# Optimization experiments

Measured on AMD Instinct MI355X. Metric: run time of the kernel, lower is better.

Reference implementation:

```python
import jax, jax.numpy as jnp
import numpy as np

B, AT, NBR, FEAT = 4, 384, 24, 128


def setup_inputs() -> dict:
    key = jax.random.key(0)
    k1, k2, k3 = jax.random.split(key, 3)
    edge_embedding = jax.random.normal(k1, (B, AT, NBR, FEAT), dtype=jnp.float32)
    nbr_idx = jax.random.randint(k2, (B, AT, NBR), 0, AT, dtype=jnp.int64)
    # periodic-cell offsets: small integers stored as float, compared exactly with ==
    cell_offset = jax.random.randint(k3, (B, AT, NBR, 3), 0, 3).astype(jnp.float32)
    return {"edge_embedding": edge_embedding, "nbr_idx": nbr_idx, "cell_offset": cell_offset}


def reference(edge_embedding, nbr_idx, cell_offset):
    # edge_embedding: (B, At, Nbr, F); nbr_idx: (B, At, Nbr) int; cell_offset: (B, At, Nbr, 3)
    Bn, At, Nbr, F = edge_embedding.shape

    # j_nbr[b,a,j,k] = nbr_idx[b, nbr_idx[b,a,j], k]  -- neighbors of atom j (j-th nbr of a)
    j_nbr = jax.vmap(lambda n: n[n])(nbr_idx)                      # (B, At, Nbr, Nbr)
    # cell_j[b,a,j,k,:] = cell_offset[b, nbr_idx[b,a,j], k, :]
    cell_j = jax.vmap(lambda c, n: c[n])(cell_offset, nbr_idx)     # (B, At, Nbr, Nbr, 3)

    # k_masked[b,a,j,i] = nbr_idx[b,a,i] with diagonal (i==j) set to -1 (exclude k==j)
    eye = jnp.eye(Nbr, dtype=bool)                                 # (Nbr, Nbr) [j, i]
    k_masked = jnp.where(eye[None, None], -1, nbr_idx[:, :, None, :])  # (B, At, Nbr, Nbr)

    # match over k: j_nbr[b,a,j,k] == k_masked[b,a,j,i]
    idx_eq = j_nbr[:, :, :, None, :] == k_masked[:, :, :, :, None]      # (B,At,Nbr,Nbr_i,Nbr_k)
    # cell check: cell_offset[b,a,i,:] == cell_j[b,a,j,k,:] for all 3 coords
    cell_eq = jnp.all(
        cell_offset[:, :, None, :, None, :] == cell_j[:, :, :, None, :, :],
        axis=-1,
    )                                                              # (B,At,Nbr,Nbr_i,Nbr_k)

    mask = jnp.any(idx_eq & cell_eq, axis=-1)                      # (B, At, Nbr_j, Nbr_i)

    # edge_jk[b,a,j,i,:] = edge_embedding[b,a,i,:] where mask else 0
    edge_jk = jnp.where(mask[..., None], edge_embedding[:, :, None, :, :],
                        jnp.zeros((), dtype=edge_embedding.dtype))
    return edge_jk
```

## Files before the change

### kernel.cpp

```cpp
#include <hip/hip_runtime.h>

#define Bb 4
#define AT 384
#define NBR 24
#define FEAT 128

__global__ __launch_bounds__(256) void GetEdgeJK_kernel(
    const float* __restrict__ edge,
    const int*   __restrict__ nbr,
    const float* __restrict__ cell,
    float*       __restrict__ out)
{
    const int blk = blockIdx.x;
    const int j   = blk % NBR;
    const int ba  = blk / NBR;
    const int b   = ba / AT;

    __shared__ int   s_nbrj[NBR];
    __shared__ float s_cellj[NBR][3];
    __shared__ int   s_mask[NBR];

    const int t = threadIdx.x;

    const int jatom = nbr[ba * NBR + j];

    if (t < NBR) {
        const int base = (b * AT + jatom) * NBR + t;
        s_nbrj[t]     = nbr[base];
        s_cellj[t][0] = cell[base * 3 + 0];
        s_cellj[t][1] = cell[base * 3 + 1];
        s_cellj[t][2] = cell[base * 3 + 2];
    }
    __syncthreads();

    if (t < NBR) {
        const int i = t;
        int m = 0;
        if (i != j) {
            const int   myidx = nbr[ba * NBR + i];
            const float c0 = cell[(ba * NBR + i) * 3 + 0];
            const float c1 = cell[(ba * NBR + i) * 3 + 1];
            const float c2 = cell[(ba * NBR + i) * 3 + 2];
            #pragma unroll
            for (int k = 0; k < NBR; ++k) {
                if (s_nbrj[k] == myidx &&
                    s_cellj[k][0] == c0 &&
                    s_cellj[k][1] == c1 &&
                    s_cellj[k][2] == c2) { m = 1; }
            }
        }
        s_mask[i] = m;
    }
    __syncthreads();

    const float4* __restrict__ erow = (const float4*)(edge + (size_t)ba * NBR * FEAT);
    float4*       __restrict__ orow = (float4*)(out + (size_t)blk * NBR * FEAT);

    const float4 zero = make_float4(0.f, 0.f, 0.f, 0.f);
    #pragma unroll
    for (int it = 0; it < 3; ++it) {
        const int q = t + it * 256;
        const int i = q >> 5;
        float4 v = zero;
        if (s_mask[i]) v = erow[q];
        orow[q] = v;
    }
}

extern "C" void kernel_launch(void* const* d_in, const int* in_sizes, int n_in,
                              void* d_out, int out_size, void* d_ws, size_t ws_size,
                              hipStream_t stream) {
    const float* edge = (const float*)d_in[0];
    const int*   nbr  = (const int*)d_in[1];
    const float* cell = (const float*)d_in[2];
    float*       out  = (float*)d_out;

    const int nblocks = Bb * AT * NBR;
    GetEdgeJK_kernel<<<nblocks, 256, 0, stream>>>(edge, nbr, cell, out);
}
```

Baseline: 88.31 us.

## Process all neighbor rows of an atom in one block to reuse loads

Changes the grid from one block per (atom, j) pair to one block per atom. Each block stages the atom's neighbor list, cell offsets and all second-hop neighbor data in shared memory, computes the full 24x24 mask, then writes all 24 output panels. This is meant to cut per-block launch and setup overhead and to reuse the edge rows across j. The cost is 24x fewer blocks with more serial work each, which lowers parallelism for what is a store-bound kernel.

```diff
diff --git a/kernel.cpp b/kernel.cpp
--- a/kernel.cpp
+++ b/kernel.cpp
@@ -4,77 +4,90 @@
 #define AT 384
 #define NBR 24
 #define FEAT 128
+#define ROWQ (FEAT / 4)
+#define PANELQ (NBR * ROWQ)
 
 __global__ __launch_bounds__(256) void GetEdgeJK_kernel(
-    const float* __restrict__ edge,
-    const int*   __restrict__ nbr,
-    const float* __restrict__ cell,
-    float*       __restrict__ out)
+    const float4* __restrict__ edge,
+    const int*    __restrict__ nbr,
+    const float*  __restrict__ cell,
+    float4*       __restrict__ out)
 {
-    const int blk = blockIdx.x;
-    const int j   = blk % NBR;
-    const int ba  = blk / NBR;
-    const int b   = ba / AT;
+    const int ba = blockIdx.x;
+    const int b  = ba / AT;
+    const int t  = threadIdx.x;
 
-    __shared__ int   s_nbrj[NBR];
-    __shared__ float s_cellj[NBR][3];
-    __shared__ int   s_mask[NBR];
-
-    const int t = threadIdx.x;
-
-    const int jatom = nbr[ba * NBR + j];
+    __shared__ int   s_nbr[NBR];
+    __shared__ float s_cell[NBR][3];
+    __shared__ int   s_nbrj[NBR][NBR];
+    __shared__ float s_cellj[NBR][NBR][3];
+    __shared__ int   s_mask[NBR * NBR];
 
     if (t < NBR) {
-        const int base = (b * AT + jatom) * NBR + t;
-        s_nbrj[t]     = nbr[base];
-        s_cellj[t][0] = cell[base * 3 + 0];
-        s_cellj[t][1] = cell[base * 3 + 1];
-        s_cellj[t][2] = cell[base * 3 + 2];
+        s_nbr[t]     = nbr[ba * NBR + t];
+        s_cell[t][0] = cell[(ba * NBR + t) * 3 + 0];
+        s_cell[t][1] = cell[(ba * NBR + t) * 3 + 1];
+        s_cell[t][2] = cell[(ba * NBR + t) * 3 + 2];
     }
     __syncthreads();
 
-    if (t < NBR) {
-        const int i = t;
-        int m = 0;
-        if (i != j) {
-            const int   myidx = nbr[ba * NBR + i];
-            const float c0 = cell[(ba * NBR + i) * 3 + 0];
-            const float c1 = cell[(ba * NBR + i) * 3 + 1];
-            const float c2 = cell[(ba * NBR + i) * 3 + 2];
-            #pragma unroll
-            for (int k = 0; k < NBR; ++k) {
-                if (s_nbrj[k] == myidx &&
-                    s_cellj[k][0] == c0 &&
-                    s_cellj[k][1] == c1 &&
-                    s_cellj[k][2] == c2) { m = 1; }
-            }
-        }
-        s_mask[i] = m;
+    for (int q = t; q < NBR * NBR; q += 256) {
+        const int j = q / NBR;
+        const int k = q % NBR;
+        const int base = (b * AT + s_nbr[j]) * NBR + k;
+        s_nbrj[j][k]     = nbr[base];
+        s_cellj[j][k][0] = cell[base * 3 + 0];
+        s_cellj[j][k][1] = cell[base * 3 + 1];
+        s_cellj[j][k][2] = cell[base * 3 + 2];
     }
     __syncthreads();
 
-    const float4* __restrict__ erow = (const float4*)(edge + (size_t)ba * NBR * FEAT);
-    float4*       __restrict__ orow = (float4*)(out + (size_t)blk * NBR * FEAT);
+    for (int p = t; p < NBR * NBR; p += 256) {
+        const int j = p / NBR;
+        const int i = p % NBR;
+        int m = 0;
+        if (i != j) {
+            const int   myidx = s_nbr[i];
+            const float c0 = s_cell[i][0];
+            const float c1 = s_cell[i][1];
+            const float c2 = s_cell[i][2];
+            #pragma unroll
+            for (int k = 0; k < NBR; ++k) {
+                if (s_nbrj[j][k] == myidx &&
+                    s_cellj[j][k][0] == c0 &&
+                    s_cellj[j][k][1] == c1 &&
+                    s_cellj[j][k][2] == c2) { m = 1; }
+            }
+        }
+        s_mask[p] = m;
+    }
+    __syncthreads();
 
+    const float4* __restrict__ erow = edge + (size_t)ba * PANELQ;
+    float4*       __restrict__ orow = out  + (size_t)ba * NBR * PANELQ;
     const float4 zero = make_float4(0.f, 0.f, 0.f, 0.f);
-    #pragma unroll
-    for (int it = 0; it < 3; ++it) {
-        const int q = t + it * 256;
-        const int i = q >> 5;
-        float4 v = zero;
-        if (s_mask[i]) v = erow[q];
-        orow[q] = v;
+
+    for (int j = 0; j < NBR; ++j) {
+        const int* __restrict__ mrow = &s_mask[j * NBR];
+        #pragma unroll
+        for (int it = 0; it < 3; ++it) {
+            const int q = it * 256 + t;
+            const int i = q >> 5;
+            float4 v = zero;
+            if (mrow[i]) v = erow[q];
+            orow[j * PANELQ + q] = v;
+        }
     }
 }
 
 extern "C" void kernel_launch(void* const* d_in, const int* in_sizes, int n_in,
                               void* d_out, int out_size, void* d_ws, size_t ws_size,
                               hipStream_t stream) {
-    const float* edge = (const float*)d_in[0];
-    const int*   nbr  = (const int*)d_in[1];
-    const float* cell = (const float*)d_in[2];
-    float*       out  = (float*)d_out;
+    const float4* edge = (const float4*)d_in[0];
+    const int*    nbr  = (const int*)d_in[1];
+    const float*  cell = (const float*)d_in[2];
+    float4*       out  = (float4*)d_out;
 
-    const int nblocks = Bb * AT * NBR;
+    const int nblocks = Bb * AT;
     GetEdgeJK_kernel<<<nblocks, 256, 0, stream>>>(edge, nbr, cell, out);
 }
```

New measurement: 100.3 us. +13.6%, slower.

## Split mask computation into separate kernel and use nontemporal bitmask-driven stores

Applied to the files above, without the earlier changes.

Computes the per-(atom, j) neighbor match mask once per atom in a dedicated kernel, packing it into a 24-bit word in workspace. A lean store kernel then reads one word and streams the output with nontemporal stores. This removes the dependent gather loads and two barriers from every output block. It adds an extra launch and a workspace round trip, and falls back to the fused kernel when workspace is insufficient.

```diff
diff --git a/kernel.cpp b/kernel.cpp
--- a/kernel.cpp
+++ b/kernel.cpp
@@ -4,8 +4,102 @@
 #define AT 384
 #define NBR 24
 #define FEAT 128
+#define ROWQ (FEAT / 4)
+#define PANELQ (NBR * ROWQ)
 
-__global__ __launch_bounds__(256) void GetEdgeJK_kernel(
+typedef float vfloat4 __attribute__((ext_vector_type(4)));
+
+__global__ __launch_bounds__(256) void mask_kernel(
+    const int*   __restrict__ nbr,
+    const float* __restrict__ cell,
+    unsigned int* __restrict__ ws)
+{
+    const int ba = blockIdx.x;
+    const int b  = ba / AT;
+    const int t  = threadIdx.x;
+
+    __shared__ int   s_nbr[NBR];
+    __shared__ float s_cell[NBR][3];
+    __shared__ int   s_nbrj[NBR][NBR];
+    __shared__ float s_cellj[NBR][NBR][3];
+    __shared__ int   s_mask[NBR * NBR];
+
+    if (t < NBR) {
+        s_nbr[t]     = nbr[ba * NBR + t];
+        s_cell[t][0] = cell[(ba * NBR + t) * 3 + 0];
+        s_cell[t][1] = cell[(ba * NBR + t) * 3 + 1];
+        s_cell[t][2] = cell[(ba * NBR + t) * 3 + 2];
+    }
+    __syncthreads();
+
+    for (int q = t; q < NBR * NBR; q += 256) {
+        const int j = q / NBR;
+        const int k = q % NBR;
+        const int base = (b * AT + s_nbr[j]) * NBR + k;
+        s_nbrj[j][k]     = nbr[base];
+        s_cellj[j][k][0] = cell[base * 3 + 0];
+        s_cellj[j][k][1] = cell[base * 3 + 1];
+        s_cellj[j][k][2] = cell[base * 3 + 2];
+    }
+    __syncthreads();
+
+    for (int p = t; p < NBR * NBR; p += 256) {
+        const int j = p / NBR;
+        const int i = p % NBR;
+        int m = 0;
+        if (i != j) {
+            const int   myidx = s_nbr[i];
+            const float c0 = s_cell[i][0];
+            const float c1 = s_cell[i][1];
+            const float c2 = s_cell[i][2];
+            #pragma unroll
+            for (int k = 0; k < NBR; ++k) {
+                if (s_nbrj[j][k] == myidx &&
+                    s_cellj[j][k][0] == c0 &&
+                    s_cellj[j][k][1] == c1 &&
+                    s_cellj[j][k][2] == c2) { m = 1; }
+            }
+        }
+        s_mask[p] = m;
+    }
+    __syncthreads();
+
+    if (t < NBR) {
+        const int j = t;
+        unsigned int w = 0;
+        #pragma unroll
+        for (int i = 0; i < NBR; ++i)
+            w |= (unsigned int)s_mask[j * NBR + i] << i;
+        ws[ba * NBR + j] = w;
+    }
+}
+
+__global__ __launch_bounds__(256) void store_kernel(
+    const vfloat4* __restrict__ edge,
+    const unsigned int* __restrict__ ws,
+    vfloat4*       __restrict__ out)
+{
+    const int blk = blockIdx.x;
+    const int ba  = blk / NBR;
+    const int t   = threadIdx.x;
+
+    const unsigned int m = ws[blk];
+
+    const vfloat4* __restrict__ erow = edge + (size_t)ba * PANELQ;
+    vfloat4*       __restrict__ orow = out  + (size_t)blk * PANELQ;
+    const vfloat4 zero = (vfloat4)(0.f);
+
+    #pragma unroll
+    for (int it = 0; it < 3; ++it) {
+        const int q = it * 256 + t;
+        const int i = q >> 5;
+        vfloat4 v = zero;
+        if ((m >> i) & 1u) v = erow[q];
+        __builtin_nontemporal_store(v, &orow[q]);
+    }
+}
+
+__global__ __launch_bounds__(256) void mono_kernel(
     const float* __restrict__ edge,
     const int*   __restrict__ nbr,
     const float* __restrict__ cell,
@@ -21,7 +115,6 @@
     __shared__ int   s_mask[NBR];
 
     const int t = threadIdx.x;
-
     const int jatom = nbr[ba * NBR + j];
 
     if (t < NBR) {
@@ -55,7 +148,6 @@
 
     const float4* __restrict__ erow = (const float4*)(edge + (size_t)ba * NBR * FEAT);
     float4*       __restrict__ orow = (float4*)(out + (size_t)blk * NBR * FEAT);
-
     const float4 zero = make_float4(0.f, 0.f, 0.f, 0.f);
     #pragma unroll
     for (int it = 0; it < 3; ++it) {
@@ -75,6 +167,13 @@
     const float* cell = (const float*)d_in[2];
     float*       out  = (float*)d_out;
 
-    const int nblocks = Bb * AT * NBR;
-    GetEdgeJK_kernel<<<nblocks, 256, 0, stream>>>(edge, nbr, cell, out);
+    const size_t need = (size_t)Bb * AT * NBR * sizeof(unsigned int);
+    if (ws_size >= need) {
+        unsigned int* ws = (unsigned int*)d_ws;
+        mask_kernel<<<Bb * AT, 256, 0, stream>>>(nbr, cell, ws);
+        store_kernel<<<Bb * AT * NBR, 256, 0, stream>>>((const vfloat4*)edge, ws,
+                                                        (vfloat4*)out);
+    } else {
+        mono_kernel<<<Bb * AT * NBR, 256, 0, stream>>>(edge, nbr, cell, out);
+    }
 }
```

Measured after the change: 95.05 us. 7.6% more time.

## Use single-wavefront blocks with ballot mask instead of shared-memory mask

Applied to the files above, without the earlier changes.

Shrinks each block to one 64-lane wavefront, so the per-row match mask is built with a wavefront ballot rather than a shared array and a second barrier. Each thread now writes 12 vector stores instead of 3, and the row's own neighbor index and cell values are loaded before the first barrier. When no row matches, the block skips the edge loads and writes only zeros. The cost is fewer threads per block, so latency hiding for this store-heavy kernel depends on how many blocks stay resident.

```diff
diff --git a/kernel.cpp b/kernel.cpp
--- a/kernel.cpp
+++ b/kernel.cpp
@@ -4,23 +4,34 @@
 #define AT 384
 #define NBR 24
 #define FEAT 128
+#define ROWQ (FEAT / 4)
+#define JROWQ (NBR * ROWQ)
 
-__global__ __launch_bounds__(256) void GetEdgeJK_kernel(
-    const float* __restrict__ edge,
-    const int*   __restrict__ nbr,
-    const float* __restrict__ cell,
-    float*       __restrict__ out)
+typedef float vfloat4 __attribute__((ext_vector_type(4)));
+
+__global__ __launch_bounds__(64) void edgejk_kernel(
+    const vfloat4* __restrict__ edge,
+    const int*     __restrict__ nbr,
+    const float*   __restrict__ cell,
+    vfloat4*       __restrict__ out)
 {
     const int blk = blockIdx.x;
     const int j   = blk % NBR;
     const int ba  = blk / NBR;
     const int b   = ba / AT;
+    const int t   = threadIdx.x;
 
     __shared__ int   s_nbrj[NBR];
     __shared__ float s_cellj[NBR][3];
-    __shared__ int   s_mask[NBR];
 
-    const int t = threadIdx.x;
+    int   myidx = -2;
+    float c0 = 0.f, c1 = 0.f, c2 = 0.f;
+    if (t < NBR) {
+        myidx = nbr[ba * NBR + t];
+        c0 = cell[(ba * NBR + t) * 3 + 0];
+        c1 = cell[(ba * NBR + t) * 3 + 1];
+        c2 = cell[(ba * NBR + t) * 3 + 2];
+    }
 
     const int jatom = nbr[ba * NBR + j];
 
@@ -33,48 +44,46 @@
     }
     __syncthreads();
 
-    if (t < NBR) {
-        const int i = t;
-        int m = 0;
-        if (i != j) {
-            const int   myidx = nbr[ba * NBR + i];
-            const float c0 = cell[(ba * NBR + i) * 3 + 0];
-            const float c1 = cell[(ba * NBR + i) * 3 + 1];
-            const float c2 = cell[(ba * NBR + i) * 3 + 2];
-            #pragma unroll
-            for (int k = 0; k < NBR; ++k) {
-                if (s_nbrj[k] == myidx &&
-                    s_cellj[k][0] == c0 &&
-                    s_cellj[k][1] == c1 &&
-                    s_cellj[k][2] == c2) { m = 1; }
-            }
+    int match = 0;
+    if (t < NBR && t != j) {
+        #pragma unroll
+        for (int k = 0; k < NBR; ++k) {
+            if (s_nbrj[k] == myidx &&
+                s_cellj[k][0] == c0 &&
+                s_cellj[k][1] == c1 &&
+                s_cellj[k][2] == c2) { match = 1; }
         }
-        s_mask[i] = m;
     }
-    __syncthreads();
+    const unsigned long long w = __ballot(match != 0);
 
-    const float4* __restrict__ erow = (const float4*)(edge + (size_t)ba * NBR * FEAT);
-    float4*       __restrict__ orow = (float4*)(out + (size_t)blk * NBR * FEAT);
+    const vfloat4* __restrict__ erow = edge + (size_t)ba * JROWQ;
+    vfloat4*       __restrict__ orow = out  + (size_t)blk * JROWQ;
+    const vfloat4 zero = (vfloat4)(0.f);
 
-    const float4 zero = make_float4(0.f, 0.f, 0.f, 0.f);
-    #pragma unroll
-    for (int it = 0; it < 3; ++it) {
-        const int q = t + it * 256;
-        const int i = q >> 5;
-        float4 v = zero;
-        if (s_mask[i]) v = erow[q];
-        orow[q] = v;
+    if (w == 0ull) {
+        #pragma unroll
+        for (int it = 0; it < 12; ++it)
+            orow[it * 64 + t] = zero;
+    } else {
+        #pragma unroll
+        for (int it = 0; it < 12; ++it) {
+            const int q = it * 64 + t;
+            const int i = q >> 5;
+            vfloat4 v = zero;
+            if ((w >> i) & 1ull) v = erow[q];
+            orow[q] = v;
+        }
     }
 }
 
 extern "C" void kernel_launch(void* const* d_in, const int* in_sizes, int n_in,
                               void* d_out, int out_size, void* d_ws, size_t ws_size,
                               hipStream_t stream) {
-    const float* edge = (const float*)d_in[0];
-    const int*   nbr  = (const int*)d_in[1];
-    const float* cell = (const float*)d_in[2];
-    float*       out  = (float*)d_out;
+    const vfloat4* edge = (const vfloat4*)d_in[0];
+    const int*     nbr  = (const int*)d_in[1];
+    const float*   cell = (const float*)d_in[2];
+    vfloat4*       out  = (vfloat4*)d_out;
 
     const int nblocks = Bb * AT * NBR;
-    GetEdgeJK_kernel<<<nblocks, 256, 0, stream>>>(edge, nbr, cell, out);
+    edgejk_kernel<<<nblocks, 64, 0, stream>>>(edge, nbr, cell, out);
 }
```

After: 94.11 us. +6.6%, slower.
